# Optimization experiments

Measured on AMD Instinct MI355X. Metric: run time of the kernel, lower is better.

Reference implementation:

```python
import jax, jax.numpy as jnp
import numpy as np

B, S, D = 2, 2048, 2048
H, KVH, HD = 16, 4, 128
N_REP = H // KVH
SCALING = HD ** -0.5
ROPE_THETA = 10000.0


def _rope_tables(batch, seq, head_dim, dtype=jnp.float32):
    inv_freq = 1.0 / (ROPE_THETA ** (jnp.arange(0, head_dim, 2, dtype=jnp.float32) / head_dim))
    t = jnp.arange(seq, dtype=jnp.float32)
    freqs = jnp.outer(t, inv_freq)                      # [S, HD/2]
    emb = jnp.concatenate([freqs, freqs], axis=-1)      # [S, HD]
    cos = jnp.broadcast_to(jnp.cos(emb), (batch, seq, head_dim)).astype(dtype)
    sin = jnp.broadcast_to(jnp.sin(emb), (batch, seq, head_dim)).astype(dtype)
    return cos, sin


def _causal_mask(batch, seq, dtype=jnp.float32):
    # HF-style additive causal mask: 0 where allowed, large negative where masked
    neg = jnp.finfo(dtype).min
    m = jnp.triu(jnp.full((seq, seq), neg, dtype=dtype), k=1)
    return jnp.broadcast_to(m[None, None], (batch, 1, seq, seq))


def setup_inputs() -> dict:
    key = jax.random.key(0)
    ks = jax.random.split(key, 8)
    w_scale = 0.02
    hidden_states = jax.random.normal(ks[0], (B, S, D), dtype=jnp.float32)
    cos, sin = _rope_tables(B, S, HD)
    attention_mask = _causal_mask(B, S)
    # Linear weights stored as [in, out] (transposed vs torch nn.Linear.weight)
    Wq = jax.random.normal(ks[1], (D, H * HD), dtype=jnp.float32) * w_scale
    bq = jax.random.normal(ks[2], (H * HD,), dtype=jnp.float32) * w_scale
    Wk = jax.random.normal(ks[3], (D, KVH * HD), dtype=jnp.float32) * w_scale
    bk = jax.random.normal(ks[4], (KVH * HD,), dtype=jnp.float32) * w_scale
    Wv = jax.random.normal(ks[5], (D, KVH * HD), dtype=jnp.float32) * w_scale
    bv = jax.random.normal(ks[6], (KVH * HD,), dtype=jnp.float32) * w_scale
    Wo = jax.random.normal(ks[7], (H * HD, D), dtype=jnp.float32) * w_scale
    return {"hidden_states": hidden_states, "cos": cos, "sin": sin,
            "attention_mask": attention_mask, "Wq": Wq, "bq": bq,
            "Wk": Wk, "bk": bk, "Wv": Wv, "bv": bv, "Wo": Wo}


def _rotate_half(x):
    x1, x2 = jnp.split(x, 2, axis=-1)
    return jnp.concatenate([-x2, x1], axis=-1)


def reference(hidden_states, cos, sin, attention_mask, Wq, bq, Wk, bk, Wv, bv, Wo):
    b, s, _ = hidden_states.shape
    # QKV projections -> [B, heads, S, HD]
    q = (hidden_states @ Wq + bq).reshape(b, s, H, HD).transpose(0, 2, 1, 3)
    k = (hidden_states @ Wk + bk).reshape(b, s, KVH, HD).transpose(0, 2, 1, 3)
    v = (hidden_states @ Wv + bv).reshape(b, s, KVH, HD).transpose(0, 2, 1, 3)
    # RoPE (cos/sin broadcast over heads via unsqueeze_dim=1)
    c = cos[:, None]  # [B,1,S,HD]
    sn = sin[:, None]
    q = q * c + _rotate_half(q) * sn
    k = k * c + _rotate_half(k) * sn
    # GQA: repeat_interleave KV heads to match query heads
    k_rep = jnp.repeat(k, N_REP, axis=1)  # [B,H,S,HD]
    v_rep = jnp.repeat(v, N_REP, axis=1)
    # Eager attention: full score matrix, fp32 softmax
    scores = jnp.einsum('bhqd,bhkd->bhqk', q, k_rep) * SCALING + attention_mask
    attn_weights = jax.nn.softmax(scores.astype(jnp.float32), axis=-1).astype(q.dtype)
    attn_out = jnp.einsum('bhqk,bhkd->bhqd', attn_weights, v_rep)
    attn_out = attn_out.transpose(0, 2, 1, 3).reshape(b, s, H * HD)
    attn_out = attn_out @ Wo
    return attn_out, attn_weights
```

## Files before the change

kernel.cpp:

```cpp
#include <hip/hip_runtime.h>

typedef unsigned short ushort_t;
typedef __attribute__((ext_vector_type(8))) short short8;
typedef __attribute__((ext_vector_type(4))) float f32x4;

#define S_  2048
#define Dm  2048
#define NH  16
#define NKV 4
#define HD_ 128
#define C2_ 0.12751879524465536f

__device__ __forceinline__ ushort_t f2bf(float f) {
  union { float f; unsigned u; } v; v.f = f;
  unsigned u = v.u;
  return (ushort_t)((u + 0x7FFFu + ((u >> 16) & 1u)) >> 16);
}
__device__ __forceinline__ ushort_t f2bf2(float f) {
  union { float f; unsigned u; } v; v.f = f;
  return (ushort_t)((v.u + 0x8000u) >> 16);
}
__device__ __forceinline__ float bf2f(ushort_t h) {
  union { unsigned u; float f; } v; v.u = ((unsigned)h) << 16;
  return v.f;
}
__device__ __forceinline__ void gl_lds16(const void* g, void* l) {
  __builtin_amdgcn_global_load_lds((const __attribute__((address_space(1))) void*)g,
                                   (__attribute__((address_space(3))) void*)l, 16, 0, 0);
}

__global__ void prep_k(const float* __restrict__ hs, ushort_t* __restrict__ hsb,
                       const float* __restrict__ Wq, const float* __restrict__ Wk,
                       const float* __restrict__ Wv, const float* __restrict__ Wo,
                       ushort_t* __restrict__ wtqkv, ushort_t* __restrict__ wto) {
  __shared__ float tile[32][33];
  const int id = blockIdx.x;
  if (id < 8192) {
    int i = id * 256 + threadIdx.x;
    float4 v = ((const float4*)hs)[i];
    union { ushort_t u[4]; uint2 v2; } o;
    o.u[0] = f2bf(v.x); o.u[1] = f2bf(v.y); o.u[2] = f2bf(v.z); o.u[3] = f2bf(v.w);
    *(uint2*)&hsb[(size_t)i * 4] = o.v2;
    return;
  }
  const int id2 = id - 8192;
  const int z = id2 >> 12, ky = (id2 >> 6) & 63, nx = id2 & 63;
  const float* src;
  ushort_t* dst;
  int N;
  switch (z) {
    case 0: src = Wq; dst = wtqkv; N = 2048; break;
    case 1: src = Wk; dst = wtqkv + (size_t)2048 * 2048; N = 512; break;
    case 2: src = Wv; dst = wtqkv + (size_t)2560 * 2048; N = 512; break;
    default: src = Wo; dst = wto; N = 2048; break;
  }
  int n0 = nx * 32, k0 = ky * 32;
  if (n0 >= N) return;
  int c = threadIdx.x & 31, r = threadIdx.x >> 5;
#pragma unroll
  for (int i = 0; i < 32; i += 8)
    tile[r + i][c] = src[(size_t)(k0 + r + i) * N + n0 + c];
  __syncthreads();
#pragma unroll
  for (int i = 0; i < 32; i += 8)
    dst[(size_t)(n0 + r + i) * 2048 + k0 + c] = f2bf(tile[c][r + i]);
}

__global__ __launch_bounds__(256, 2) void gemm_qkv_k(
    const ushort_t* __restrict__ A, const ushort_t* __restrict__ Bt, ushort_t* __restrict__ C,
// ... 96 lines not shown
        }
    }
#pragma unroll
    for (int ni = 0; ni < 4; ni++)
#pragma unroll
      for (int r = 0; r < 4; r++) {
        int row = m0 + wr * 64 + mi * 16 + lg * 4 + r;
        int col = n0 + wc * 64 + ni * 16 + lr;
        ushort_t hv = f2bf(vv[ni][r]);
        C[(size_t)row * N + col] = hv;
        if (isV) {
          int colL = wc * 64 + ni * 16 + lr;
          int rowL = wr * 64 + mi * 16 + lg * 4 + r;
          smem[colL * 128 + (rowL ^ ((colL & 7) << 4))] = hv;
        }
      }
  }
  if (isV) {
    __syncthreads();
    const int kvh = (n0 - 2560) >> 7;
    const int b = m0 >> 11, s0v = m0 & 2047;
    const size_t vbase = (size_t)(b * 4 + kvh) * 128;
#pragma unroll
    for (int j = 0; j < 8; j++) {
      int cid = j * 256 + t;
      int d = cid >> 4, sc = cid & 15;
      int rowStart = (sc * 8) ^ ((d & 7) << 4);
      short8 v8 = *(const short8*)&smem[d * 128 + rowStart];
      *(short8*)&vt[(vbase + d) * S_ + s0v + sc * 8] = v8;
    }
  }
}

__global__ __launch_bounds__(256, 2) void attn_k(
    const ushort_t* __restrict__ qkv, const ushort_t* __restrict__ vt,
    float* __restrict__ linv_g, ushort_t* __restrict__ attnO, float* __restrict__ outW) {
  __shared__ ushort_t lK[2][64 * 128];
  __shared__ ushort_t lV[2][128 * 64];
  __shared__ ushort_t lP[4][16 * 64];
  const int nid = (blockIdx.x & 7) * 64 + (blockIdx.x >> 3);
  const int pairI = nid & 15, h = (nid >> 4) & 15, b = nid >> 8;
  const int kvh = h >> 2;
  const int t = threadIdx.x, w = t >> 6, l = t & 63, lr = l & 15, lg = l >> 4;
  ushort_t* lPw = lP[w];

  auto stage = [&](int kt, int bufi) {
#pragma unroll
    for (int c = 0; c < 4; c++) {
      int row = c * 16 + (t >> 4), sl = t & 15;
      gl_lds16(qkv + (size_t)(b * S_ + kt * 64 + row) * 3072 + 2048 + kvh * HD_ +
                   ((sl ^ (row & 15)) << 3),
               &lK[bufi][c * 2048 + w * 512]);
    }
#pragma unroll
    for (int c = 0; c < 4; c++) {
      int row = c * 32 + (t >> 3), sl = t & 7;
      gl_lds16(vt + (size_t)((b * 4 + kvh) * 128 + row) * S_ + kt * 64 +
                   ((sl ^ (row & 7)) << 3),
               &lV[bufi][c * 2048 + w * 512]);
    }
  };

  for (int sel = 0; sel < 2; sel++) {
    const int qt = sel ? (31 - pairI) : pairI;
    const int qw = qt * 64 + w * 16;
    const int nkt = qt + 1;

    short8 qf[4];
#pragma unroll
    for (int kc = 0; kc < 4; kc++)
      qf[kc] = *(const short8*)&qkv[(size_t)(b * S_ + qw + lr) * 3072 + h * HD_ + kc * 32 + lg * 8];

    float lsum[4];
    f32x4 o[8];
#pragma unroll
    for (int r = 0; r < 4; r++) lsum[r] = 0.f;
#pragma unroll
    for (int dj = 0; dj < 8; dj++) o[dj] = (f32x4){0.f, 0.f, 0.f, 0.f};

    stage(0, 0);
    for (int kt = 0; kt < nkt; kt++) {
      const int cur = kt & 1;
      if (kt + 1 < nkt) {
        stage(kt + 1, cur ^ 1);
        asm volatile("s_waitcnt vmcnt(8)" ::: "memory");
      } else {
        asm volatile("s_waitcnt vmcnt(0)" ::: "memory");
      }
      __builtin_amdgcn_s_barrier();

      f32x4 s[4];
#pragma unroll
      for (int ni = 0; ni < 4; ni++) s[ni] = (f32x4){0.f, 0.f, 0.f, 0.f};
      __builtin_amdgcn_s_setprio(1);
#pragma unroll
      for (int kc = 0; kc < 4; kc++) {
        short8 kf[4];
#pragma unroll
        for (int ni = 0; ni < 4; ni++) {
          int row = ni * 16 + lr;
          kf[ni] = *(const short8*)((const char*)lK[cur] + row * 256 +
                                    (((kc * 4 + lg) ^ (row & 15)) << 4));
        }
#pragma unroll
        for (int ni = 0; ni < 4; ni++)
          s[ni] = __builtin_amdgcn_mfma_f32_16x16x32_bf16(qf[kc], kf[ni], s[ni], 0, 0, 0);
      }
      __builtin_amdgcn_s_setprio(0);

      if (kt == nkt - 1) {
#pragma unroll
        for (int ni = 0; ni < 4; ni++)
#pragma unroll
          for (int r = 0; r < 4; r++) {
            float p = exp2f(s[ni][r] * C2_);
            int colg = kt * 64 + ni * 16 + lr;
            int rowg = qw + lg * 4 + r;
            if (colg > rowg) p = 0.f;
            lsum[r] += p;
            int rowl = lg * 4 + r, col = ni * 16 + lr;
            lPw[rowl * 64 + (((col >> 3) ^ (rowl & 7)) << 3) + (col & 7)] = f2bf2(p);
          }
      } else {
#pragma unroll
        for (int ni = 0; ni < 4; ni++)
#pragma unroll
          for (int r = 0; r < 4; r++) {
            float p = exp2f(s[ni][r] * C2_);
            lsum[r] += p;
            int rowl = lg * 4 + r, col = ni * 16 + lr;
            lPw[rowl * 64 + (((col >> 3) ^ (rowl & 7)) << 3) + (col & 7)] = f2bf2(p);
          }
      }

      __builtin_amdgcn_s_setprio(1);
#pragma unroll
      for (int kc = 0; kc < 2; kc++) {
        short8 pa;
        {
          int row = lr;
          pa = *(const short8*)((const char*)lPw + row * 128 + (((kc * 4 + lg) ^ (row & 7)) << 4));
        }
#pragma unroll
        for (int dj = 0; dj < 8; dj++) {
          int row = dj * 16 + lr;
          short8 vb = *(const short8*)((const char*)lV[cur] + row * 128 +
                                       (((kc * 4 + lg) ^ (row & 7)) << 4));
          o[dj] = __builtin_amdgcn_mfma_f32_16x16x32_bf16(pa, vb, o[dj], 0, 0, 0);
        }
      }
      __builtin_amdgcn_s_setprio(0);
      __builtin_amdgcn_s_barrier();
    }

    float inv_l[4];
#pragma unroll
    for (int r = 0; r < 4; r++) {
      float sum = lsum[r];
#pragma unroll
      for (int off = 1; off < 16; off <<= 1) sum += __shfl_xor(sum, off);
      inv_l[r] = 1.f / sum;
      if (lr == 0) linv_g[(size_t)(b * NH + h) * S_ + qw + lg * 4 + r] = inv_l[r];
    }
#pragma unroll
    for (int dj = 0; dj < 8; dj++)
#pragma unroll
      for (int r = 0; r < 4; r++) {
        int rowg = b * S_ + qw + lg * 4 + r;
        int colg = h * HD_ + dj * 16 + lr;
        attnO[(size_t)rowg * Dm + colg] = f2bf(o[dj][r] * inv_l[r]);
      }

    {
      const int zc0 = nkt * 64;
      const int zn = (S_ - zc0) >> 2;
      f32x4 z = {0.f, 0.f, 0.f, 0.f};
      const int bh = b * NH + h;
      for (int rr = 0; rr < 16; rr++) {
        f32x4* base = (f32x4*)&outW[((size_t)bh * S_ + qw + rr) * S_ + zc0];
        for (int cc = l; cc < zn; cc += 64) __builtin_nontemporal_store(z, base + cc);
      }
    }
  }
}

__global__ __launch_bounds__(256, 2) void tail_k(
    const ushort_t* __restrict__ A, const ushort_t* __restrict__ Bt, float* __restrict__ outO,
    const ushort_t* __restrict__ qkv, const float* __restrict__ linv,
    float* __restrict__ outW) {
  __shared__ ushort_t sh[2][64 * 128];
  const int bx = blockIdx.x;
  const int t = threadIdx.x;
  const int w = t >> 6, l = t & 63, lr = l & 15, lg = l >> 4;

  if (bx < 512) {
    const int N = 2048, K = 2048;
    const int nid = (bx & 7) * 64 + (bx >> 3);
    const int n0 = (nid & 15) * 128, m0 = (nid >> 4) * 128;
    const int wr = w >> 1, wc = w & 1;
    const int srow = t >> 2, ssl = t & 3;

    auto stageG = [&](int kt, int bufi) {
      int r0 = srow, r1 = srow + 64;
      gl_lds16(A + (size_t)(m0 + r0) * K + kt + ((ssl ^ ((r0 >> 1) & 3)) << 3), &sh[bufi][w * 512]);
      gl_lds16(A + (size_t)(m0 + r1) * K + kt + ((ssl ^ ((r1 >> 1) & 3)) << 3),
               &sh[bufi][2048 + w * 512]);
      gl_lds16(Bt + (size_t)(n0 + r0) * K + kt + ((ssl ^ ((r0 >> 1) & 3)) << 3),
               &sh[bufi][4096 + w * 512]);
      gl_lds16(Bt + (size_t)(n0 + r1) * K + kt + ((ssl ^ ((r1 >> 1) & 3)) << 3),
               &sh[bufi][4096 + 2048 + w * 512]);
    };

    f32x4 acc[4][4];
#pragma unroll
    for (int i = 0; i < 4; i++)
#pragma unroll
      for (int j = 0; j < 4; j++) acc[i][j] = (f32x4){0.f, 0.f, 0.f, 0.f};

    stageG(0, 0);
    const int nit = K / 32;
    for (int it = 0; it < nit; it++) {
      const int cur = it & 1;
      if (it + 1 < nit) {
        stageG((it + 1) * 32, cur ^ 1);
        asm volatile("s_waitcnt vmcnt(4)" ::: "memory");
      } else {
        asm volatile("s_waitcnt vmcnt(0)" ::: "memory");
      }
      __builtin_amdgcn_s_barrier();
      short8 af[4], bfr[4];
#pragma unroll
      for (int mi = 0; mi < 4; mi++) {
        int row = wr * 64 + mi * 16 + lr;
        af[mi] =
            *(const short8*)((const char*)&sh[cur][0] + row * 64 + ((lg ^ ((row >> 1) & 3)) << 4));
      }
#pragma unroll
      for (int ni = 0; ni < 4; ni++) {
        int row = wc * 64 + ni * 16 + lr;
        bfr[ni] = *(const short8*)((const char*)&sh[cur][4096] + row * 64 +
                                   ((lg ^ ((row >> 1) & 3)) << 4));
      }
#pragma unroll
      for (int mi = 0; mi < 4; mi++)
#pragma unroll
        for (int ni = 0; ni < 4; ni++)
          acc[mi][ni] =
              __builtin_amdgcn_mfma_f32_16x16x32_bf16(af[mi], bfr[ni], acc[mi][ni], 0, 0, 0);
      __builtin_amdgcn_s_barrier();
    }
#pragma unroll
    for (int mi = 0; mi < 4; mi++)
#pragma unroll
      for (int ni = 0; ni < 4; ni++)
#pragma unroll
        for (int r = 0; r < 4; r++) {
          int row = m0 + wr * 64 + mi * 16 + lg * 4 + r;
          int col = n0 + wc * 64 + ni * 16 + lr;
          outO[(size_t)row * N + col] = acc[mi][ni][r];
        }
    return;
  }

  const int lin = bx - 512;
  const int nid = (lin & 7) * 64 + (lin >> 3);
  const int bh = nid >> 4;
  const int pi = nid & 15;
  const int b = bh >> 4, h = bh & 15;
  const int kvh = h >> 2;

  auto stageK = [&](int kt, int bufi) {
#pragma unroll
    for (int c = 0; c < 4; c++) {
      int row = c * 16 + (t >> 4), sl = t & 15;
      gl_lds16(qkv + (size_t)(b * S_ + kt * 64 + row) * 3072 + 2048 + kvh * HD_ +
                   ((sl ^ (row & 15)) << 3),
               &sh[bufi][c * 2048 + w * 512]);
    }
  };

  for (int sel = 0; sel < 2; sel++) {
    const int qt = sel ? (31 - pi) : pi;
    const int qw = qt * 64 + w * 16;
    const int nkt = qt + 1;

    short8 qf[4];
#pragma unroll
    for (int kc = 0; kc < 4; kc++)
      qf[kc] = *(const short8*)&qkv[(size_t)(b * S_ + qw + lr) * 3072 + h * HD_ + kc * 32 + lg * 8];

    float invr[4];
#pragma unroll
    for (int r = 0; r < 4; r++) invr[r] = linv[(size_t)bh * S_ + qw + lg * 4 + r];

    stageK(0, 0);
    for (int kt = 0; kt < nkt; kt++) {
      const int cur = kt & 1;
      if (kt + 1 < nkt) {
        stageK(kt + 1, cur ^ 1);
        asm volatile("s_waitcnt vmcnt(4)" ::: "memory");
      } else {
        asm volatile("s_waitcnt vmcnt(0)" ::: "memory");
      }
      __builtin_amdgcn_s_barrier();

      f32x4 s[4];
#pragma unroll
      for (int ni = 0; ni < 4; ni++) s[ni] = (f32x4){0.f, 0.f, 0.f, 0.f};
#pragma unroll
      for (int kc = 0; kc < 4; kc++) {
        short8 kf[4];
#pragma unroll
        for (int ni = 0; ni < 4; ni++) {
          int row = ni * 16 + lr;
          kf[ni] = *(const short8*)((const char*)sh[cur] + row * 256 +
                                    (((kc * 4 + lg) ^ (row & 15)) << 4));
        }
#pragma unroll
        for (int ni = 0; ni < 4; ni++)
          s[ni] = __builtin_amdgcn_mfma_f32_16x16x32_bf16(qf[kc], kf[ni], s[ni], 0, 0, 0);
      }

      const bool diag = (kt == nkt - 1);
#pragma unroll
      for (int ni = 0; ni < 4; ni++)
#pragma unroll
        for (int r = 0; r < 4; r++) {
          int colg = kt * 64 + ni * 16 + lr;
          int rowg = qw + lg * 4 + r;
          float p = exp2f(s[ni][r] * C2_) * invr[r];
          if (diag && colg > rowg) p = 0.f;
          outW[((size_t)bh * S_ + rowg) * S_ + colg] = p;
        }
      __builtin_amdgcn_s_barrier();
    }
  }
}

extern "C" void kernel_launch(void* const* d_in, const int* in_sizes, int n_in,
                              void* d_out, int out_size, void* d_ws, size_t ws_size,
                              hipStream_t stream) {
  const float* hs   = (const float*)d_in[0];
  const float* cosT = (const float*)d_in[1];
  const float* sinT = (const float*)d_in[2];
  const float* Wq = (const float*)d_in[4];
  const float* bq = (const float*)d_in[5];
  const float* Wk = (const float*)d_in[6];
  const float* bk = (const float*)d_in[7];
  const float* Wv = (const float*)d_in[8];
  const float* bv = (const float*)d_in[9];
  const float* Wo = (const float*)d_in[10];

  char* ws = (char*)d_ws;
  ushort_t* hsb   = (ushort_t*)(ws);
  ushort_t* wtqkv = (ushort_t*)(ws + 16777216);
  ushort_t* wto   = (ushort_t*)(ws + 29360128);
  ushort_t* qkv   = (ushort_t*)(ws + 37748736);
  ushort_t* vt    = (ushort_t*)(ws + 62914560);
  float*    linv  = (float*)(ws + 67108864);
  ushort_t* attn  = (ushort_t*)(ws);

  float* outO = (float*)d_out;
  float* outW = outO + (size_t)8388608;

  prep_k<<<8192 + 16384, 256, 0, stream>>>(hs, hsb, Wq, Wk, Wv, Wo, wtqkv, wto);
  gemm_qkv_k<<<768, 256, 0, stream>>>(hsb, wtqkv, qkv, bq, bk, bv, cosT, sinT, vt);
  attn_k<<<512, 256, 0, stream>>>(qkv, vt, linv, attn, outW);
  tail_k<<<1024, 256, 0, stream>>>(attn, wto, outO, qkv, linv, outW);
}
```

Measured before the change: 306.9 us.

## Fuse attention, weight write and output GEMM into one persistent kernel with flags

Merges the attention kernel and the tail kernel (output projection GEMM plus attention-weight write) into one launch. Blocks take work items from an atomic ticket counter, and consumers wait on per-tile completion flags, so the weight write and the Wo GEMM can start while attention is still running. Attention work is split into one block per query tile, heaviest first, instead of paired tiles. This aims to remove the launch boundary and the tail imbalance, but adds spin-waits, atomics and a reset of the sync counters in prep_k.

```diff
diff --git a/kernel.cpp b/kernel.cpp
--- a/kernel.cpp
+++ b/kernel.cpp
@@ -32,9 +32,14 @@
 __global__ void prep_k(const float* __restrict__ hs, ushort_t* __restrict__ hsb,
                        const float* __restrict__ Wq, const float* __restrict__ Wk,
                        const float* __restrict__ Wv, const float* __restrict__ Wo,
-                       ushort_t* __restrict__ wtqkv, ushort_t* __restrict__ wto) {
+                       ushort_t* __restrict__ wtqkv, ushort_t* __restrict__ wto,
+                       int* __restrict__ syncp) {
   __shared__ float tile[32][33];
   const int id = blockIdx.x;
+  if (id >= 24576) {
+    for (int i = threadIdx.x; i < 1057; i += 256) syncp[i] = 0;
+    return;
+  }
   if (id < 8192) {
     int i = id * 256 + threadIdx.x;
     float4 v = ((const float4*)hs)[i];
@@ -197,39 +202,47 @@
   }
 }
 
-__global__ __launch_bounds__(256, 2) void attn_k(
+__global__ __launch_bounds__(256, 2) void fused_k(
     const ushort_t* __restrict__ qkv, const ushort_t* __restrict__ vt,
-    float* __restrict__ linv_g, ushort_t* __restrict__ attnO, float* __restrict__ outW) {
-  __shared__ ushort_t lK[2][64 * 128];
-  __shared__ ushort_t lV[2][128 * 64];
-  __shared__ ushort_t lP[4][16 * 64];
-  const int nid = (blockIdx.x & 7) * 64 + (blockIdx.x >> 3);
-  const int pairI = nid & 15, h = (nid >> 4) & 15, b = nid >> 8;
-  const int kvh = h >> 2;
-  const int t = threadIdx.x, w = t >> 6, l = t & 63, lr = l & 15, lg = l >> 4;
-  ushort_t* lPw = lP[w];
-
-  auto stage = [&](int kt, int bufi) {
-#pragma unroll
-    for (int c = 0; c < 4; c++) {
-      int row = c * 16 + (t >> 4), sl = t & 15;
-      gl_lds16(qkv + (size_t)(b * S_ + kt * 64 + row) * 3072 + 2048 + kvh * HD_ +
-                   ((sl ^ (row & 15)) << 3),
-               &lK[bufi][c * 2048 + w * 512]);
-    }
-#pragma unroll
-    for (int c = 0; c < 4; c++) {
-      int row = c * 32 + (t >> 3), sl = t & 7;
-      gl_lds16(vt + (size_t)((b * 4 + kvh) * 128 + row) * S_ + kt * 64 +
-                   ((sl ^ (row & 7)) << 3),
-               &lV[bufi][c * 2048 + w * 512]);
-    }
-  };
-
-  for (int sel = 0; sel < 2; sel++) {
-    const int qt = sel ? (31 - pairI) : pairI;
+    float* __restrict__ linv_g, ushort_t* __restrict__ attnO, float* __restrict__ outW,
+    const ushort_t* __restrict__ wto, float* __restrict__ outO, int* __restrict__ sync) {
+  __shared__ ushort_t smem[36864];
+  __shared__ int s_tk;
+  const int t = threadIdx.x;
+  if (t == 0)
+    s_tk = __hip_atomic_fetch_add(&sync[0], 1, __ATOMIC_RELAXED, __HIP_MEMORY_SCOPE_AGENT);
+  __syncthreads();
+  const int bx = s_tk;
+  int* flin = sync + 1;
+  int* fmt = sync + 1025;
+  const int w = t >> 6, l = t & 63, lr = l & 15, lg = l >> 4;
+
+  if (bx < 1024) {
+    ushort_t* lK = smem;
+    ushort_t* lV = smem + 16384;
+    ushort_t* lPw = smem + 32768 + w * 1024;
+    const int qt = 31 - (bx >> 5);
+    const int bh = bx & 31;
+    const int b = bh >> 4, h = bh & 15, kvh = h >> 2;
     const int qw = qt * 64 + w * 16;
     const int nkt = qt + 1;
+
+    auto stage = [&](int kt, int bufi) {
+#pragma unroll
+      for (int c = 0; c < 4; c++) {
+        int row = c * 16 + (t >> 4), sl = t & 15;
+        gl_lds16(qkv + (size_t)(b * S_ + kt * 64 + row) * 3072 + 2048 + kvh * HD_ +
+                     ((sl ^ (row & 15)) << 3),
+                 &lK[bufi * 8192 + c * 2048 + w * 512]);
+      }
+#pragma unroll
+      for (int c = 0; c < 4; c++) {
+        int row = c * 32 + (t >> 3), sl = t & 7;
+        gl_lds16(vt + (size_t)((b * 4 + kvh) * 128 + row) * S_ + kt * 64 +
+                     ((sl ^ (row & 7)) << 3),
+                 &lV[bufi * 8192 + c * 2048 + w * 512]);
+      }
+    };
 
     short8 qf[4];
 #pragma unroll
@@ -264,7 +277,7 @@
 #pragma unroll
         for (int ni = 0; ni < 4; ni++) {
           int row = ni * 16 + lr;
-          kf[ni] = *(const short8*)((const char*)lK[cur] + row * 256 +
+          kf[ni] = *(const short8*)((const char*)(lK + cur * 8192) + row * 256 +
                                     (((kc * 4 + lg) ^ (row & 15)) << 4));
         }
 #pragma unroll
@@ -309,7 +322,7 @@
 #pragma unroll
         for (int dj = 0; dj < 8; dj++) {
           int row = dj * 16 + lr;
-          short8 vb = *(const short8*)((const char*)lV[cur] + row * 128 +
+          short8 vb = *(const short8*)((const char*)(lV + cur * 8192) + row * 128 +
                                        (((kc * 4 + lg) ^ (row & 7)) << 4));
           o[dj] = __builtin_amdgcn_mfma_f32_16x16x32_bf16(pa, vb, o[dj], 0, 0, 0);
         }
@@ -325,7 +338,7 @@
 #pragma unroll
       for (int off = 1; off < 16; off <<= 1) sum += __shfl_xor(sum, off);
       inv_l[r] = 1.f / sum;
-      if (lr == 0) linv_g[(size_t)(b * NH + h) * S_ + qw + lg * 4 + r] = inv_l[r];
+      if (lr == 0) linv_g[(size_t)bh * S_ + qw + lg * 4 + r] = inv_l[r];
     }
 #pragma unroll
     for (int dj = 0; dj < 8; dj++)
@@ -340,115 +353,48 @@
       const int zc0 = nkt * 64;
       const int zn = (S_ - zc0) >> 2;
       f32x4 z = {0.f, 0.f, 0.f, 0.f};
-      const int bh = b * NH + h;
       for (int rr = 0; rr < 16; rr++) {
         f32x4* base = (f32x4*)&outW[((size_t)bh * S_ + qw + rr) * S_ + zc0];
         for (int cc = l; cc < zn; cc += 64) __builtin_nontemporal_store(z, base + cc);
       }
     }
-  }
-}
-
-__global__ __launch_bounds__(256, 2) void tail_k(
-    const ushort_t* __restrict__ A, const ushort_t* __restrict__ Bt, float* __restrict__ outO,
-    const ushort_t* __restrict__ qkv, const float* __restrict__ linv,
-    float* __restrict__ outW) {
-  __shared__ ushort_t sh[2][64 * 128];
-  const int bx = blockIdx.x;
-  const int t = threadIdx.x;
-  const int w = t >> 6, l = t & 63, lr = l & 15, lg = l >> 4;
-
-  if (bx < 512) {
-    const int N = 2048, K = 2048;
-    const int nid = (bx & 7) * 64 + (bx >> 3);
-    const int n0 = (nid & 15) * 128, m0 = (nid >> 4) * 128;
-    const int wr = w >> 1, wc = w & 1;
-    const int srow = t >> 2, ssl = t & 3;
-
-    auto stageG = [&](int kt, int bufi) {
-      int r0 = srow, r1 = srow + 64;
-      gl_lds16(A + (size_t)(m0 + r0) * K + kt + ((ssl ^ ((r0 >> 1) & 3)) << 3), &sh[bufi][w * 512]);
-      gl_lds16(A + (size_t)(m0 + r1) * K + kt + ((ssl ^ ((r1 >> 1) & 3)) << 3),
-               &sh[bufi][2048 + w * 512]);
-      gl_lds16(Bt + (size_t)(n0 + r0) * K + kt + ((ssl ^ ((r0 >> 1) & 3)) << 3),
-               &sh[bufi][4096 + w * 512]);
-      gl_lds16(Bt + (size_t)(n0 + r1) * K + kt + ((ssl ^ ((r1 >> 1) & 3)) << 3),
-               &sh[bufi][4096 + 2048 + w * 512]);
-    };
-
-    f32x4 acc[4][4];
-#pragma unroll
-    for (int i = 0; i < 4; i++)
-#pragma unroll
-      for (int j = 0; j < 4; j++) acc[i][j] = (f32x4){0.f, 0.f, 0.f, 0.f};
-
-    stageG(0, 0);
-    const int nit = K / 32;
-    for (int it = 0; it < nit; it++) {
-      const int cur = it & 1;
-      if (it + 1 < nit) {
-        stageG((it + 1) * 32, cur ^ 1);
-        asm volatile("s_waitcnt vmcnt(4)" ::: "memory");
-      } else {
-        asm volatile("s_waitcnt vmcnt(0)" ::: "memory");
-      }
-      __builtin_amdgcn_s_barrier();
-      short8 af[4], bfr[4];
-#pragma unroll
-      for (int mi = 0; mi < 4; mi++) {
-        int row = wr * 64 + mi * 16 + lr;
-        af[mi] =
-            *(const short8*)((const char*)&sh[cur][0] + row * 64 + ((lg ^ ((row >> 1) & 3)) << 4));
-      }
-#pragma unroll
-      for (int ni = 0; ni < 4; ni++) {
-        int row = wc * 64 + ni * 16 + lr;
-        bfr[ni] = *(const short8*)((const char*)&sh[cur][4096] + row * 64 +
-                                   ((lg ^ ((row >> 1) & 3)) << 4));
-      }
-#pragma unroll
-      for (int mi = 0; mi < 4; mi++)
-#pragma unroll
-        for (int ni = 0; ni < 4; ni++)
-          acc[mi][ni] =
-              __builtin_amdgcn_mfma_f32_16x16x32_bf16(af[mi], bfr[ni], acc[mi][ni], 0, 0, 0);
-      __builtin_amdgcn_s_barrier();
-    }
-#pragma unroll
-    for (int mi = 0; mi < 4; mi++)
-#pragma unroll
-      for (int ni = 0; ni < 4; ni++)
-#pragma unroll
-        for (int r = 0; r < 4; r++) {
-          int row = m0 + wr * 64 + mi * 16 + lg * 4 + r;
-          int col = n0 + wc * 64 + ni * 16 + lr;
-          outO[(size_t)row * N + col] = acc[mi][ni][r];
-        }
+
+    __threadfence();
+    __syncthreads();
+    if (t == 0) {
+      __hip_atomic_fetch_add(&flin[bh * 32 + qt], 1, __ATOMIC_RELEASE, __HIP_MEMORY_SCOPE_AGENT);
+      __hip_atomic_fetch_add(&fmt[b * 16 + (qt >> 1)], 1, __ATOMIC_RELEASE,
+                             __HIP_MEMORY_SCOPE_AGENT);
+    }
     return;
   }
 
-  const int lin = bx - 512;
-  const int nid = (lin & 7) * 64 + (lin >> 3);
-  const int bh = nid >> 4;
-  const int pi = nid & 15;
-  const int b = bh >> 4, h = bh & 15;
-  const int kvh = h >> 2;
-
-  auto stageK = [&](int kt, int bufi) {
-#pragma unroll
-    for (int c = 0; c < 4; c++) {
-      int row = c * 16 + (t >> 4), sl = t & 15;
-      gl_lds16(qkv + (size_t)(b * S_ + kt * 64 + row) * 3072 + 2048 + kvh * HD_ +
-                   ((sl ^ (row & 15)) << 3),
-               &sh[bufi][c * 2048 + w * 512]);
-    }
-  };
-
-  for (int sel = 0; sel < 2; sel++) {
-    const int qt = sel ? (31 - pi) : pi;
+  if (bx < 2048) {
+    const int bx2 = bx - 1024;
+    const int qt = ((bx2 >> 5) + 16) & 31;
+    const int bh = bx2 & 31;
+    const int b = bh >> 4, h = bh & 15, kvh = h >> 2;
     const int qw = qt * 64 + w * 16;
     const int nkt = qt + 1;
 
+    if (t == 0) {
+      while (__hip_atomic_load(&flin[bh * 32 + qt], __ATOMIC_ACQUIRE,
+                               __HIP_MEMORY_SCOPE_AGENT) < 1)
+        __builtin_amdgcn_s_sleep(16);
+    }
+    __syncthreads();
+    __threadfence();
+
+    auto stageK = [&](int kt, int bufi) {
+#pragma unroll
+      for (int c = 0; c < 4; c++) {
+        int row = c * 16 + (t >> 4), sl = t & 15;
+        gl_lds16(qkv + (size_t)(b * S_ + kt * 64 + row) * 3072 + 2048 + kvh * HD_ +
+                     ((sl ^ (row & 15)) << 3),
+                 &smem[bufi * 8192 + c * 2048 + w * 512]);
+      }
+    };
+
     short8 qf[4];
 #pragma unroll
     for (int kc = 0; kc < 4; kc++)
@@ -456,7 +402,7 @@
 
     float invr[4];
 #pragma unroll
-    for (int r = 0; r < 4; r++) invr[r] = linv[(size_t)bh * S_ + qw + lg * 4 + r];
+    for (int r = 0; r < 4; r++) invr[r] = linv_g[(size_t)bh * S_ + qw + lg * 4 + r];
 
     stageK(0, 0);
     for (int kt = 0; kt < nkt; kt++) {
@@ -478,7 +424,7 @@
 #pragma unroll
         for (int ni = 0; ni < 4; ni++) {
           int row = ni * 16 + lr;
-          kf[ni] = *(const short8*)((const char*)sh[cur] + row * 256 +
+          kf[ni] = *(const short8*)((const char*)(smem + cur * 8192) + row * 256 +
                                     (((kc * 4 + lg) ^ (row & 15)) << 4));
         }
 #pragma unroll
@@ -499,7 +445,83 @@
         }
       __builtin_amdgcn_s_barrier();
     }
-  }
+    return;
+  }
+
+  const int bx3 = bx - 2048;
+  const int nid = (bx3 & 7) * 64 + (bx3 >> 3);
+  const int n0 = (nid & 15) * 128, m0 = (nid >> 4) * 128;
+  const int N = 2048, K = 2048;
+  const int wr = w >> 1, wc = w & 1;
+  const int srow = t >> 2, ssl = t & 3;
+  const ushort_t* Agm = attnO;
+
+  if (t == 0) {
+    while (__hip_atomic_load(&fmt[nid >> 4], __ATOMIC_ACQUIRE, __HIP_MEMORY_SCOPE_AGENT) < 32)
+      __builtin_amdgcn_s_sleep(16);
+  }
+  __syncthreads();
+  __threadfence();
+
+  auto stageG = [&](int kt, int bufi) {
+    int r0 = srow, r1 = srow + 64;
+    gl_lds16(Agm + (size_t)(m0 + r0) * K + kt + ((ssl ^ ((r0 >> 1) & 3)) << 3),
+             &smem[bufi * 8192 + w * 512]);
+    gl_lds16(Agm + (size_t)(m0 + r1) * K + kt + ((ssl ^ ((r1 >> 1) & 3)) << 3),
+             &smem[bufi * 8192 + 2048 + w * 512]);
+    gl_lds16(wto + (size_t)(n0 + r0) * K + kt + ((ssl ^ ((r0 >> 1) & 3)) << 3),
+             &smem[bufi * 8192 + 4096 + w * 512]);
+    gl_lds16(wto + (size_t)(n0 + r1) * K + kt + ((ssl ^ ((r1 >> 1) & 3)) << 3),
+             &smem[bufi * 8192 + 4096 + 2048 + w * 512]);
+  };
+
+  f32x4 acc[4][4];
+#pragma unroll
+  for (int i = 0; i < 4; i++)
+#pragma unroll
+    for (int j = 0; j < 4; j++) acc[i][j] = (f32x4){0.f, 0.f, 0.f, 0.f};
+
+  stageG(0, 0);
+  const int nit = K / 32;
+  for (int it = 0; it < nit; it++) {
+    const int cur = it & 1;
+    if (it + 1 < nit) {
+      stageG((it + 1) * 32, cur ^ 1);
+      asm volatile("s_waitcnt vmcnt(4)" ::: "memory");
+    } else {
+      asm volatile("s_waitcnt vmcnt(0)" ::: "memory");
+    }
+    __builtin_amdgcn_s_barrier();
+    short8 af[4], bfr[4];
+#pragma unroll
+    for (int mi = 0; mi < 4; mi++) {
+      int row = wr * 64 + mi * 16 + lr;
+      af[mi] = *(const short8*)((const char*)(smem + cur * 8192) + row * 64 +
+                                ((lg ^ ((row >> 1) & 3)) << 4));
+    }
+#pragma unroll
+    for (int ni = 0; ni < 4; ni++) {
+      int row = wc * 64 + ni * 16 + lr;
+      bfr[ni] = *(const short8*)((const char*)(smem + cur * 8192 + 4096) + row * 64 +
+                                 ((lg ^ ((row >> 1) & 3)) << 4));
+    }
+#pragma unroll
+    for (int mi = 0; mi < 4; mi++)
+#pragma unroll
+      for (int ni = 0; ni < 4; ni++)
+        acc[mi][ni] = __builtin_amdgcn_mfma_f32_16x16x32_bf16(af[mi], bfr[ni], acc[mi][ni], 0, 0, 0);
+    __builtin_amdgcn_s_barrier();
+  }
+#pragma unroll
+  for (int mi = 0; mi < 4; mi++)
+#pragma unroll
+    for (int ni = 0; ni < 4; ni++)
+#pragma unroll
+      for (int r = 0; r < 4; r++) {
+        int row = m0 + wr * 64 + mi * 16 + lg * 4 + r;
+        int col = n0 + wc * 64 + ni * 16 + lr;
+        outO[(size_t)row * N + col] = acc[mi][ni][r];
+      }
 }
 
 extern "C" void kernel_launch(void* const* d_in, const int* in_sizes, int n_in,
@@ -523,13 +545,13 @@
   ushort_t* qkv   = (ushort_t*)(ws + 37748736);
   ushort_t* vt    = (ushort_t*)(ws + 62914560);
   float*    linv  = (float*)(ws + 67108864);
+  int*      syncp = (int*)(ws + 67371008);
   ushort_t* attn  = (ushort_t*)(ws);
 
   float* outO = (float*)d_out;
   float* outW = outO + (size_t)8388608;
 
-  prep_k<<<8192 + 16384, 256, 0, stream>>>(hs, hsb, Wq, Wk, Wv, Wo, wtqkv, wto);
+  prep_k<<<24577, 256, 0, stream>>>(hs, hsb, Wq, Wk, Wv, Wo, wtqkv, wto, syncp);
   gemm_qkv_k<<<768, 256, 0, stream>>>(hsb, wtqkv, qkv, bq, bk, bv, cosT, sinT, vt);
-  attn_k<<<512, 256, 0, stream>>>(qkv, vt, linv, attn, outW);
-  tail_k<<<1024, 256, 0, stream>>>(attn, wto, outO, qkv, linv, outW);
-}
+  fused_k<<<2560, 256, 0, stream>>>(qkv, vt, linv, attn, outW, wto, outO, syncp);
+}
```

New measurement: 764.8 us. +149.2%, slower.

## Split attention into per-q-tile blocks, drop LDS double buffering for higher occupancy

Applied to the files above, without the earlier changes.

The attention kernel now launches one block per (batch, head, query tile), 1024 blocks, instead of pairing a short and a long causal tile in each of 512 blocks. The K/V LDS buffers go from double to single buffering, which halves shared memory. The launch-bounds hint rises from 2 to 4 blocks per CU to raise occupancy. The trade-off is that loads no longer overlap with compute inside a block, since each iteration waits on vmcnt(0). It also drops the causal load-balancing pairing, so latency hiding now relies on other resident blocks.

```diff
diff --git a/kernel.cpp b/kernel.cpp
--- a/kernel.cpp
+++ b/kernel.cpp
@@ -197,154 +197,146 @@
   }
 }
 
-__global__ __launch_bounds__(256, 2) void attn_k(
+__global__ __launch_bounds__(256, 4) void attn_k(
     const ushort_t* __restrict__ qkv, const ushort_t* __restrict__ vt,
     float* __restrict__ linv_g, ushort_t* __restrict__ attnO, float* __restrict__ outW) {
-  __shared__ ushort_t lK[2][64 * 128];
-  __shared__ ushort_t lV[2][128 * 64];
+  __shared__ ushort_t lK[64 * 128];
+  __shared__ ushort_t lV[128 * 64];
   __shared__ ushort_t lP[4][16 * 64];
-  const int nid = (blockIdx.x & 7) * 64 + (blockIdx.x >> 3);
-  const int pairI = nid & 15, h = (nid >> 4) & 15, b = nid >> 8;
+  const int bx = blockIdx.x;
+  const int qt = bx & 31;
+  const int bh = bx >> 5;
+  const int b = bh >> 4, h = bh & 15;
   const int kvh = h >> 2;
   const int t = threadIdx.x, w = t >> 6, l = t & 63, lr = l & 15, lg = l >> 4;
   ushort_t* lPw = lP[w];
 
-  auto stage = [&](int kt, int bufi) {
+  const int qw = qt * 64 + w * 16;
+  const int nkt = qt + 1;
+
+  auto stage = [&](int kt) {
 #pragma unroll
     for (int c = 0; c < 4; c++) {
       int row = c * 16 + (t >> 4), sl = t & 15;
       gl_lds16(qkv + (size_t)(b * S_ + kt * 64 + row) * 3072 + 2048 + kvh * HD_ +
                    ((sl ^ (row & 15)) << 3),
-               &lK[bufi][c * 2048 + w * 512]);
+               &lK[c * 2048 + w * 512]);
     }
 #pragma unroll
     for (int c = 0; c < 4; c++) {
       int row = c * 32 + (t >> 3), sl = t & 7;
       gl_lds16(vt + (size_t)((b * 4 + kvh) * 128 + row) * S_ + kt * 64 +
                    ((sl ^ (row & 7)) << 3),
-               &lV[bufi][c * 2048 + w * 512]);
+               &lV[c * 2048 + w * 512]);
     }
   };
 
-  for (int sel = 0; sel < 2; sel++) {
-    const int qt = sel ? (31 - pairI) : pairI;
-    const int qw = qt * 64 + w * 16;
-    const int nkt = qt + 1;
-
-    short8 qf[4];
-#pragma unroll
-    for (int kc = 0; kc < 4; kc++)
-      qf[kc] = *(const short8*)&qkv[(size_t)(b * S_ + qw + lr) * 3072 + h * HD_ + kc * 32 + lg * 8];
-
-    float lsum[4];
-    f32x4 o[8];
-#pragma unroll
-    for (int r = 0; r < 4; r++) lsum[r] = 0.f;
-#pragma unroll
-    for (int dj = 0; dj < 8; dj++) o[dj] = (f32x4){0.f, 0.f, 0.f, 0.f};
-
-    stage(0, 0);
-    for (int kt = 0; kt < nkt; kt++) {
-      const int cur = kt & 1;
-      if (kt + 1 < nkt) {
-        stage(kt + 1, cur ^ 1);
-        asm volatile("s_waitcnt vmcnt(8)" ::: "memory");
-      } else {
-        asm volatile("s_waitcnt vmcnt(0)" ::: "memory");
-      }
-      __builtin_amdgcn_s_barrier();
-
-      f32x4 s[4];
-#pragma unroll
-      for (int ni = 0; ni < 4; ni++) s[ni] = (f32x4){0.f, 0.f, 0.f, 0.f};
-      __builtin_amdgcn_s_setprio(1);
-#pragma unroll
-      for (int kc = 0; kc < 4; kc++) {
-        short8 kf[4];
-#pragma unroll
-        for (int ni = 0; ni < 4; ni++) {
-          int row = ni * 16 + lr;
-          kf[ni] = *(const short8*)((const char*)lK[cur] + row * 256 +
-                                    (((kc * 4 + lg) ^ (row & 15)) << 4));
-        }
-#pragma unroll
-        for (int ni = 0; ni < 4; ni++)
-          s[ni] = __builtin_amdgcn_mfma_f32_16x16x32_bf16(qf[kc], kf[ni], s[ni], 0, 0, 0);
-      }
-      __builtin_amdgcn_s_setprio(0);
-
-      if (kt == nkt - 1) {
-#pragma unroll
-        for (int ni = 0; ni < 4; ni++)
-#pragma unroll
-          for (int r = 0; r < 4; r++) {
-            float p = exp2f(s[ni][r] * C2_);
-            int colg = kt * 64 + ni * 16 + lr;
-            int rowg = qw + lg * 4 + r;
-            if (colg > rowg) p = 0.f;
-            lsum[r] += p;
-            int rowl = lg * 4 + r, col = ni * 16 + lr;
-            lPw[rowl * 64 + (((col >> 3) ^ (rowl & 7)) << 3) + (col & 7)] = f2bf2(p);
-          }
-      } else {
-#pragma unroll
-        for (int ni = 0; ni < 4; ni++)
-#pragma unroll
-          for (int r = 0; r < 4; r++) {
-            float p = exp2f(s[ni][r] * C2_);
-            lsum[r] += p;
-            int rowl = lg * 4 + r, col = ni * 16 + lr;
-            lPw[rowl * 64 + (((col >> 3) ^ (rowl & 7)) << 3) + (col & 7)] = f2bf2(p);
-          }
-      }
-
-      __builtin_amdgcn_s_setprio(1);
-#pragma unroll
-      for (int kc = 0; kc < 2; kc++) {
-        short8 pa;
-        {
-          int row = lr;
-          pa = *(const short8*)((const char*)lPw + row * 128 + (((kc * 4 + lg) ^ (row & 7)) << 4));
-        }
-#pragma unroll
-        for (int dj = 0; dj < 8; dj++) {
-          int row = dj * 16 + lr;
-          short8 vb = *(const short8*)((const char*)lV[cur] + row * 128 +
-                                       (((kc * 4 + lg) ^ (row & 7)) << 4));
-          o[dj] = __builtin_amdgcn_mfma_f32_16x16x32_bf16(pa, vb, o[dj], 0, 0, 0);
-        }
-      }
-      __builtin_amdgcn_s_setprio(0);
-      __builtin_amdgcn_s_barrier();
-    }
-
-    float inv_l[4];
+  short8 qf[4];
+#pragma unroll
+  for (int kc = 0; kc < 4; kc++)
+    qf[kc] = *(const short8*)&qkv[(size_t)(b * S_ + qw + lr) * 3072 + h * HD_ + kc * 32 + lg * 8];
+
+  float lsum[4];
+  f32x4 o[8];
+#pragma unroll
+  for (int r = 0; r < 4; r++) lsum[r] = 0.f;
+#pragma unroll
+  for (int dj = 0; dj < 8; dj++) o[dj] = (f32x4){0.f, 0.f, 0.f, 0.f};
+
+  for (int kt = 0; kt < nkt; kt++) {
+    stage(kt);
+    asm volatile("s_waitcnt vmcnt(0)" ::: "memory");
+    __builtin_amdgcn_s_barrier();
+
+    f32x4 s[4];
+#pragma unroll
+    for (int ni = 0; ni < 4; ni++) s[ni] = (f32x4){0.f, 0.f, 0.f, 0.f};
+    __builtin_amdgcn_s_setprio(1);
+#pragma unroll
+    for (int kc = 0; kc < 4; kc++) {
+      short8 kf[4];
+#pragma unroll
+      for (int ni = 0; ni < 4; ni++) {
+        int row = ni * 16 + lr;
+        kf[ni] = *(const short8*)((const char*)lK + row * 256 +
+                                  (((kc * 4 + lg) ^ (row & 15)) << 4));
+      }
+#pragma unroll
+      for (int ni = 0; ni < 4; ni++)
+        s[ni] = __builtin_amdgcn_mfma_f32_16x16x32_bf16(qf[kc], kf[ni], s[ni], 0, 0, 0);
+    }
+    __builtin_amdgcn_s_setprio(0);
+
+    if (kt == nkt - 1) {
+#pragma unroll
+      for (int ni = 0; ni < 4; ni++)
+#pragma unroll
+        for (int r = 0; r < 4; r++) {
+          float p = exp2f(s[ni][r] * C2_);
+          int colg = kt * 64 + ni * 16 + lr;
+          int rowg = qw + lg * 4 + r;
+          if (colg > rowg) p = 0.f;
+          lsum[r] += p;
+          int rowl = lg * 4 + r, col = ni * 16 + lr;
+          lPw[rowl * 64 + (((col >> 3) ^ (rowl & 7)) << 3) + (col & 7)] = f2bf2(p);
+        }
+    } else {
+#pragma unroll
+      for (int ni = 0; ni < 4; ni++)
+#pragma unroll
+        for (int r = 0; r < 4; r++) {
+          float p = exp2f(s[ni][r] * C2_);
+          lsum[r] += p;
+          int rowl = lg * 4 + r, col = ni * 16 + lr;
+          lPw[rowl * 64 + (((col >> 3) ^ (rowl & 7)) << 3) + (col & 7)] = f2bf2(p);
+        }
+    }
+
+    __builtin_amdgcn_s_setprio(1);
+#pragma unroll
+    for (int kc = 0; kc < 2; kc++) {
+      short8 pa;
+      {
+        int row = lr;
+        pa = *(const short8*)((const char*)lPw + row * 128 + (((kc * 4 + lg) ^ (row & 7)) << 4));
+      }
+#pragma unroll
+      for (int dj = 0; dj < 8; dj++) {
+        int row = dj * 16 + lr;
+        short8 vb = *(const short8*)((const char*)lV + row * 128 +
+                                     (((kc * 4 + lg) ^ (row & 7)) << 4));
+        o[dj] = __builtin_amdgcn_mfma_f32_16x16x32_bf16(pa, vb, o[dj], 0, 0, 0);
+      }
+    }
+    __builtin_amdgcn_s_setprio(0);
+    __builtin_amdgcn_s_barrier();
+  }
+
+  float inv_l[4];
+#pragma unroll
+  for (int r = 0; r < 4; r++) {
+    float sum = lsum[r];
+#pragma unroll
+    for (int off = 1; off < 16; off <<= 1) sum += __shfl_xor(sum, off);
+    inv_l[r] = 1.f / sum;
+    if (lr == 0) linv_g[(size_t)bh * S_ + qw + lg * 4 + r] = inv_l[r];
+  }
+#pragma unroll
+  for (int dj = 0; dj < 8; dj++)
 #pragma unroll
     for (int r = 0; r < 4; r++) {
-      float sum = lsum[r];
-#pragma unroll
-      for (int off = 1; off < 16; off <<= 1) sum += __shfl_xor(sum, off);
-      inv_l[r] = 1.f / sum;
-      if (lr == 0) linv_g[(size_t)(b * NH + h) * S_ + qw + lg * 4 + r] = inv_l[r];
-    }
-#pragma unroll
-    for (int dj = 0; dj < 8; dj++)
-#pragma unroll
-      for (int r = 0; r < 4; r++) {
-        int rowg = b * S_ + qw + lg * 4 + r;
-        int colg = h * HD_ + dj * 16 + lr;
-        attnO[(size_t)rowg * Dm + colg] = f2bf(o[dj][r] * inv_l[r]);
-      }
-
-    {
-      const int zc0 = nkt * 64;
-      const int zn = (S_ - zc0) >> 2;
-      f32x4 z = {0.f, 0.f, 0.f, 0.f};
-      const int bh = b * NH + h;
-      for (int rr = 0; rr < 16; rr++) {
-        f32x4* base = (f32x4*)&outW[((size_t)bh * S_ + qw + rr) * S_ + zc0];
-        for (int cc = l; cc < zn; cc += 64) __builtin_nontemporal_store(z, base + cc);
-      }
+      int rowg = b * S_ + qw + lg * 4 + r;
+      int colg = h * HD_ + dj * 16 + lr;
+      attnO[(size_t)rowg * Dm + colg] = f2bf(o[dj][r] * inv_l[r]);
+    }
+
+  {
+    const int zc0 = nkt * 64;
+    const int zn = (S_ - zc0) >> 2;
+    f32x4 z = {0.f, 0.f, 0.f, 0.f};
+    for (int rr = 0; rr < 16; rr++) {
+      f32x4* base = (f32x4*)&outW[((size_t)bh * S_ + qw + rr) * S_ + zc0];
+      for (int cc = l; cc < zn; cc += 64) __builtin_nontemporal_store(z, base + cc);
     }
   }
 }
@@ -530,6 +522,6 @@
 
   prep_k<<<8192 + 16384, 256, 0, stream>>>(hs, hsb, Wq, Wk, Wv, Wo, wtqkv, wto);
   gemm_qkv_k<<<768, 256, 0, stream>>>(hsb, wtqkv, qkv, bq, bk, bv, cosT, sinT, vt);
-  attn_k<<<512, 256, 0, stream>>>(qkv, vt, linv, attn, outW);
+  attn_k<<<1024, 256, 0, stream>>>(qkv, vt, linv, attn, outW);
   tail_k<<<1024, 256, 0, stream>>>(attn, wto, outO, qkv, linv, outW);
 }
```

Result: slower. 339.7 us (+10.7%).

## Fuse attention-weight recompute pass into attention kernel, drop linv buffer

Applied to the files above, without the earlier changes.

The second pass that recomputes QK^T scores and writes normalized attention probabilities moves from the tail kernel into the attention kernel, running right after the PV pass with the inverse row sums still in registers. This removes the global linv round trip and leaves the tail kernel as a pure output-projection GEMM. The cost is a longer attention kernel: 512 blocks now do both passes serially. Before, that second pass ran concurrently with the Wo GEMM inside tail_k, so load balance and overlap across the GPU change.

```diff
diff --git a/kernel.cpp b/kernel.cpp
--- a/kernel.cpp
+++ b/kernel.cpp
@@ -199,7 +199,7 @@
 
 __global__ __launch_bounds__(256, 2) void attn_k(
     const ushort_t* __restrict__ qkv, const ushort_t* __restrict__ vt,
-    float* __restrict__ linv_g, ushort_t* __restrict__ attnO, float* __restrict__ outW) {
+    ushort_t* __restrict__ attnO, float* __restrict__ outW) {
   __shared__ ushort_t lK[2][64 * 128];
   __shared__ ushort_t lV[2][128 * 64];
   __shared__ ushort_t lP[4][16 * 64];
@@ -209,7 +209,7 @@
   const int t = threadIdx.x, w = t >> 6, l = t & 63, lr = l & 15, lg = l >> 4;
   ushort_t* lPw = lP[w];
 
-  auto stage = [&](int kt, int bufi) {
+  auto stageKV = [&](int kt, int bufi) {
 #pragma unroll
     for (int c = 0; c < 4; c++) {
       int row = c * 16 + (t >> 4), sl = t & 15;
@@ -225,6 +225,15 @@
                &lV[bufi][c * 2048 + w * 512]);
     }
   };
+  auto stageK = [&](int kt, int bufi) {
+#pragma unroll
+    for (int c = 0; c < 4; c++) {
+      int row = c * 16 + (t >> 4), sl = t & 15;
+      gl_lds16(qkv + (size_t)(b * S_ + kt * 64 + row) * 3072 + 2048 + kvh * HD_ +
+                   ((sl ^ (row & 15)) << 3),
+               &lK[bufi][c * 2048 + w * 512]);
+    }
+  };
 
   for (int sel = 0; sel < 2; sel++) {
     const int qt = sel ? (31 - pairI) : pairI;
@@ -243,11 +252,11 @@
 #pragma unroll
     for (int dj = 0; dj < 8; dj++) o[dj] = (f32x4){0.f, 0.f, 0.f, 0.f};
 
-    stage(0, 0);
+    stageKV(0, 0);
     for (int kt = 0; kt < nkt; kt++) {
       const int cur = kt & 1;
       if (kt + 1 < nkt) {
-        stage(kt + 1, cur ^ 1);
+        stageKV(kt + 1, cur ^ 1);
         asm volatile("s_waitcnt vmcnt(8)" ::: "memory");
       } else {
         asm volatile("s_waitcnt vmcnt(0)" ::: "memory");
@@ -325,7 +334,6 @@
 #pragma unroll
       for (int off = 1; off < 16; off <<= 1) sum += __shfl_xor(sum, off);
       inv_l[r] = 1.f / sum;
-      if (lr == 0) linv_g[(size_t)(b * NH + h) * S_ + qw + lg * 4 + r] = inv_l[r];
     }
 #pragma unroll
     for (int dj = 0; dj < 8; dj++)
@@ -346,160 +354,126 @@
         for (int cc = l; cc < zn; cc += 64) __builtin_nontemporal_store(z, base + cc);
       }
     }
+
+    {
+      const int bh = b * NH + h;
+      stageK(0, 0);
+      for (int kt = 0; kt < nkt; kt++) {
+        const int cur = kt & 1;
+        if (kt + 1 < nkt) {
+          stageK(kt + 1, cur ^ 1);
+          asm volatile("s_waitcnt vmcnt(4)" ::: "memory");
+        } else {
+          asm volatile("s_waitcnt vmcnt(0)" ::: "memory");
+        }
+        __builtin_amdgcn_s_barrier();
+
+        f32x4 s[4];
+#pragma unroll
+        for (int ni = 0; ni < 4; ni++) s[ni] = (f32x4){0.f, 0.f, 0.f, 0.f};
+        __builtin_amdgcn_s_setprio(1);
+#pragma unroll
+        for (int kc = 0; kc < 4; kc++) {
+          short8 kf[4];
+#pragma unroll
+          for (int ni = 0; ni < 4; ni++) {
+            int row = ni * 16 + lr;
+            kf[ni] = *(const short8*)((const char*)lK[cur] + row * 256 +
+                                      (((kc * 4 + lg) ^ (row & 15)) << 4));
+          }
+#pragma unroll
+          for (int ni = 0; ni < 4; ni++)
+            s[ni] = __builtin_amdgcn_mfma_f32_16x16x32_bf16(qf[kc], kf[ni], s[ni], 0, 0, 0);
+        }
+        __builtin_amdgcn_s_setprio(0);
+
+        const bool diag = (kt == nkt - 1);
+#pragma unroll
+        for (int ni = 0; ni < 4; ni++)
+#pragma unroll
+          for (int r = 0; r < 4; r++) {
+            int colg = kt * 64 + ni * 16 + lr;
+            int rowg = qw + lg * 4 + r;
+            float p = exp2f(s[ni][r] * C2_) * inv_l[r];
+            if (diag && colg > rowg) p = 0.f;
+            outW[((size_t)bh * S_ + rowg) * S_ + colg] = p;
+          }
+        __builtin_amdgcn_s_barrier();
+      }
+    }
   }
 }
 
 __global__ __launch_bounds__(256, 2) void tail_k(
-    const ushort_t* __restrict__ A, const ushort_t* __restrict__ Bt, float* __restrict__ outO,
-    const ushort_t* __restrict__ qkv, const float* __restrict__ linv,
-    float* __restrict__ outW) {
+    const ushort_t* __restrict__ A, const ushort_t* __restrict__ Bt, float* __restrict__ outO) {
   __shared__ ushort_t sh[2][64 * 128];
-  const int bx = blockIdx.x;
   const int t = threadIdx.x;
   const int w = t >> 6, l = t & 63, lr = l & 15, lg = l >> 4;
-
-  if (bx < 512) {
-    const int N = 2048, K = 2048;
-    const int nid = (bx & 7) * 64 + (bx >> 3);
-    const int n0 = (nid & 15) * 128, m0 = (nid >> 4) * 128;
-    const int wr = w >> 1, wc = w & 1;
-    const int srow = t >> 2, ssl = t & 3;
-
-    auto stageG = [&](int kt, int bufi) {
-      int r0 = srow, r1 = srow + 64;
-      gl_lds16(A + (size_t)(m0 + r0) * K + kt + ((ssl ^ ((r0 >> 1) & 3)) << 3), &sh[bufi][w * 512]);
-      gl_lds16(A + (size_t)(m0 + r1) * K + kt + ((ssl ^ ((r1 >> 1) & 3)) << 3),
-               &sh[bufi][2048 + w * 512]);
-      gl_lds16(Bt + (size_t)(n0 + r0) * K + kt + ((ssl ^ ((r0 >> 1) & 3)) << 3),
-               &sh[bufi][4096 + w * 512]);
-      gl_lds16(Bt + (size_t)(n0 + r1) * K + kt + ((ssl ^ ((r1 >> 1) & 3)) << 3),
-               &sh[bufi][4096 + 2048 + w * 512]);
-    };
-
-    f32x4 acc[4][4];
-#pragma unroll
-    for (int i = 0; i < 4; i++)
-#pragma unroll
-      for (int j = 0; j < 4; j++) acc[i][j] = (f32x4){0.f, 0.f, 0.f, 0.f};
-
-    stageG(0, 0);
-    const int nit = K / 32;
-    for (int it = 0; it < nit; it++) {
-      const int cur = it & 1;
-      if (it + 1 < nit) {
-        stageG((it + 1) * 32, cur ^ 1);
-        asm volatile("s_waitcnt vmcnt(4)" ::: "memory");
-      } else {
-        asm volatile("s_waitcnt vmcnt(0)" ::: "memory");
-      }
-      __builtin_amdgcn_s_barrier();
-      short8 af[4], bfr[4];
-#pragma unroll
-      for (int mi = 0; mi < 4; mi++) {
-        int row = wr * 64 + mi * 16 + lr;
-        af[mi] =
-            *(const short8*)((const char*)&sh[cur][0] + row * 64 + ((lg ^ ((row >> 1) & 3)) << 4));
-      }
-#pragma unroll
-      for (int ni = 0; ni < 4; ni++) {
-        int row = wc * 64 + ni * 16 + lr;
-        bfr[ni] = *(const short8*)((const char*)&sh[cur][4096] + row * 64 +
-                                   ((lg ^ ((row >> 1) & 3)) << 4));
-      }
-#pragma unroll
-      for (int mi = 0; mi < 4; mi++)
-#pragma unroll
-        for (int ni = 0; ni < 4; ni++)
-          acc[mi][ni] =
-              __builtin_amdgcn_mfma_f32_16x16x32_bf16(af[mi], bfr[ni], acc[mi][ni], 0, 0, 0);
-      __builtin_amdgcn_s_barrier();
+  const int N = 2048, K = 2048;
+  const int nid = (blockIdx.x & 7) * 64 + (blockIdx.x >> 3);
+  const int n0 = (nid & 15) * 128, m0 = (nid >> 4) * 128;
+  const int wr = w >> 1, wc = w & 1;
+  const int srow = t >> 2, ssl = t & 3;
+
+  auto stageG = [&](int kt, int bufi) {
+    int r0 = srow, r1 = srow + 64;
+    gl_lds16(A + (size_t)(m0 + r0) * K + kt + ((ssl ^ ((r0 >> 1) & 3)) << 3), &sh[bufi][w * 512]);
+    gl_lds16(A + (size_t)(m0 + r1) * K + kt + ((ssl ^ ((r1 >> 1) & 3)) << 3),
+             &sh[bufi][2048 + w * 512]);
+    gl_lds16(Bt + (size_t)(n0 + r0) * K + kt + ((ssl ^ ((r0 >> 1) & 3)) << 3),
+             &sh[bufi][4096 + w * 512]);
+    gl_lds16(Bt + (size_t)(n0 + r1) * K + kt + ((ssl ^ ((r1 >> 1) & 3)) << 3),
+             &sh[bufi][4096 + 2048 + w * 512]);
+  };
+
+  f32x4 acc[4][4];
+#pragma unroll
+  for (int i = 0; i < 4; i++)
+#pragma unroll
+    for (int j = 0; j < 4; j++) acc[i][j] = (f32x4){0.f, 0.f, 0.f, 0.f};
+
+  stageG(0, 0);
+  const int nit = K / 32;
+  for (int it = 0; it < nit; it++) {
+    const int cur = it & 1;
+    if (it + 1 < nit) {
+      stageG((it + 1) * 32, cur ^ 1);
+      asm volatile("s_waitcnt vmcnt(4)" ::: "memory");
+    } else {
+      asm volatile("s_waitcnt vmcnt(0)" ::: "memory");
+    }
+    __builtin_amdgcn_s_barrier();
+    short8 af[4], bfr[4];
+#pragma unroll
+    for (int mi = 0; mi < 4; mi++) {
+      int row = wr * 64 + mi * 16 + lr;
+      af[mi] =
+          *(const short8*)((const char*)&sh[cur][0] + row * 64 + ((lg ^ ((row >> 1) & 3)) << 4));
+    }
+#pragma unroll
+    for (int ni = 0; ni < 4; ni++) {
+      int row = wc * 64 + ni * 16 + lr;
+      bfr[ni] = *(const short8*)((const char*)&sh[cur][4096] + row * 64 +
+                                 ((lg ^ ((row >> 1) & 3)) << 4));
     }
 #pragma unroll
     for (int mi = 0; mi < 4; mi++)
 #pragma unroll
       for (int ni = 0; ni < 4; ni++)
-#pragma unroll
-        for (int r = 0; r < 4; r++) {
-          int row = m0 + wr * 64 + mi * 16 + lg * 4 + r;
-          int col = n0 + wc * 64 + ni * 16 + lr;
-          outO[(size_t)row * N + col] = acc[mi][ni][r];
-        }
-    return;
-  }
-
-  const int lin = bx - 512;
-  const int nid = (lin & 7) * 64 + (lin >> 3);
-  const int bh = nid >> 4;
-  const int pi = nid & 15;
-  const int b = bh >> 4, h = bh & 15;
-  const int kvh = h >> 2;
-
-  auto stageK = [&](int kt, int bufi) {
-#pragma unroll
-    for (int c = 0; c < 4; c++) {
-      int row = c * 16 + (t >> 4), sl = t & 15;
-      gl_lds16(qkv + (size_t)(b * S_ + kt * 64 + row) * 3072 + 2048 + kvh * HD_ +
-                   ((sl ^ (row & 15)) << 3),
-               &sh[bufi][c * 2048 + w * 512]);
-    }
-  };
-
-  for (int sel = 0; sel < 2; sel++) {
-    const int qt = sel ? (31 - pi) : pi;
-    const int qw = qt * 64 + w * 16;
-    const int nkt = qt + 1;
-
-    short8 qf[4];
-#pragma unroll
-    for (int kc = 0; kc < 4; kc++)
-      qf[kc] = *(const short8*)&qkv[(size_t)(b * S_ + qw + lr) * 3072 + h * HD_ + kc * 32 + lg * 8];
-
-    float invr[4];
-#pragma unroll
-    for (int r = 0; r < 4; r++) invr[r] = linv[(size_t)bh * S_ + qw + lg * 4 + r];
-
-    stageK(0, 0);
-    for (int kt = 0; kt < nkt; kt++) {
-      const int cur = kt & 1;
-      if (kt + 1 < nkt) {
-        stageK(kt + 1, cur ^ 1);
-        asm volatile("s_waitcnt vmcnt(4)" ::: "memory");
-      } else {
-        asm volatile("s_waitcnt vmcnt(0)" ::: "memory");
-      }
-      __builtin_amdgcn_s_barrier();
-
-      f32x4 s[4];
-#pragma unroll
-      for (int ni = 0; ni < 4; ni++) s[ni] = (f32x4){0.f, 0.f, 0.f, 0.f};
-#pragma unroll
-      for (int kc = 0; kc < 4; kc++) {
-        short8 kf[4];
-#pragma unroll
-        for (int ni = 0; ni < 4; ni++) {
-          int row = ni * 16 + lr;
-          kf[ni] = *(const short8*)((const char*)sh[cur] + row * 256 +
-                                    (((kc * 4 + lg) ^ (row & 15)) << 4));
-        }
-#pragma unroll
-        for (int ni = 0; ni < 4; ni++)
-          s[ni] = __builtin_amdgcn_mfma_f32_16x16x32_bf16(qf[kc], kf[ni], s[ni], 0, 0, 0);
-      }
-
-      const bool diag = (kt == nkt - 1);
-#pragma unroll
-      for (int ni = 0; ni < 4; ni++)
-#pragma unroll
-        for (int r = 0; r < 4; r++) {
-          int colg = kt * 64 + ni * 16 + lr;
-          int rowg = qw + lg * 4 + r;
-          float p = exp2f(s[ni][r] * C2_) * invr[r];
-          if (diag && colg > rowg) p = 0.f;
-          outW[((size_t)bh * S_ + rowg) * S_ + colg] = p;
-        }
-      __builtin_amdgcn_s_barrier();
-    }
-  }
+        acc[mi][ni] =
+            __builtin_amdgcn_mfma_f32_16x16x32_bf16(af[mi], bfr[ni], acc[mi][ni], 0, 0, 0);
+    __builtin_amdgcn_s_barrier();
+  }
+#pragma unroll
+  for (int mi = 0; mi < 4; mi++)
+#pragma unroll
+    for (int ni = 0; ni < 4; ni++)
+#pragma unroll
+      for (int r = 0; r < 4; r++) {
+        int row = m0 + wr * 64 + mi * 16 + lg * 4 + r;
+        int col = n0 + wc * 64 + ni * 16 + lr;
+        outO[(size_t)row * N + col] = acc[mi][ni][r];
+      }
 }
 
 extern "C" void kernel_launch(void* const* d_in, const int* in_sizes, int n_in,
@@ -522,7 +496,6 @@
   ushort_t* wto   = (ushort_t*)(ws + 29360128);
   ushort_t* qkv   = (ushort_t*)(ws + 37748736);
   ushort_t* vt    = (ushort_t*)(ws + 62914560);
-  float*    linv  = (float*)(ws + 67108864);
   ushort_t* attn  = (ushort_t*)(ws);
 
   float* outO = (float*)d_out;
@@ -530,6 +503,6 @@
 
   prep_k<<<8192 + 16384, 256, 0, stream>>>(hs, hsb, Wq, Wk, Wv, Wo, wtqkv, wto);
   gemm_qkv_k<<<768, 256, 0, stream>>>(hsb, wtqkv, qkv, bq, bk, bv, cosT, sinT, vt);
-  attn_k<<<512, 256, 0, stream>>>(qkv, vt, linv, attn, outW);
-  tail_k<<<1024, 256, 0, stream>>>(attn, wto, outO, qkv, linv, outW);
-}
+  attn_k<<<512, 256, 0, stream>>>(qkv, vt, attn, outW);
+  tail_k<<<512, 256, 0, stream>>>(attn, wto, outO);
+}
```

Measured after the change: 299.2 us, median of 3. 2.5% less time.
